# Optimization experiments

Hardware: AMD Instinct MI355X
Metric: run time of the kernel (lower is better)

## Reference

```python
import math
import jax, jax.numpy as jnp
import numpy as np

EPS = 1e-5
NUM_HEADER = 2


def pos_encoding(C, T, dtype):
    i = jnp.arange(C)
    exp = -((i - (i % 2)).astype(dtype) / C)
    freqs = jnp.power(jnp.asarray(10000.0, dtype), exp)[:, None]      # [C,1]
    phases = ((i % 2).astype(dtype) * (np.pi / 2))[:, None]           # [C,1]
    pos = jnp.arange(T, dtype=dtype)[None, :]                         # [1,T]
    return jnp.sin(pos * freqs + phases)                              # [C,T]


def layernorm2d(x, g, b):
    # LayerNorm over (C,T) jointly, per batch element (nn.LayerNorm([C, length]))
    mu = jnp.mean(x, axis=(1, 2), keepdims=True)
    var = jnp.mean((x - mu) ** 2, axis=(1, 2), keepdims=True)
    return (x - mu) * jax.lax.rsqrt(var + EPS) * g[None] + b[None]


def dsconv(x, dw_w, dw_b, pw_w, pw_b):
    # depthwise conv1d (groups=C, 'same' padding for odd k) + pointwise 1x1
    C = x.shape[1]
    k = dw_w.shape[-1]
    y = jax.lax.conv_general_dilated(
        x, dw_w[:, None, :], (1,), [(k // 2, k // 2)],
        dimension_numbers=('NCH', 'OIH', 'NCH'), feature_group_count=C)
    y = y + dw_b[None, :, None]
    y = jnp.einsum('bct,oc->bot', y, pw_w) + pw_b[None, :, None]
    return y


def attention(x, mask, Wq, Wk, Wv, Wo):
    # Faithful to source bug: all heads use Wqs[1]/Wks[1]/Wvs[1] -> identical heads.
    xt = jnp.transpose(x, (0, 2, 1))          # [B,T,C]
    C = xt.shape[-1]
    dk = C / NUM_HEADER
    q = xt @ Wq                               # [B,T,dk]
    k_ = xt @ Wk
    v = xt @ Wv
    s = jnp.einsum('bqd,bkd->bqk', q, k_) * (1.0 / math.sqrt(dk))
    hmask = mask[:, None, :]                  # mask over keys
    s = s * hmask + (1 - hmask) * (-1e30)
    a = jax.nn.softmax(s, axis=2) * mask[:, :, None]
    head = a @ v                              # [B,T,dk]
    heads = jnp.tile(head, (1, 1, NUM_HEADER))  # concat of identical heads
    out = heads @ Wo                          # [B,T,C]
    return jnp.transpose(out, (0, 2, 1))      # [B,C,T]


def setup_inputs() -> dict:
    key = jax.random.key(0)
    B, C, T = 16, 128, 1024
    NCONV, K = 4, 7
    dk = C // NUM_HEADER
    ks = jax.random.split(key, 12)
    inp = {
        'x': jax.random.normal(ks[0], (B, C, T), jnp.float32),
        'mask': jnp.ones((B, T), jnp.float32),
        'dw_w': jax.random.normal(ks[1], (NCONV, C, K), jnp.float32) * math.sqrt(2.0 / K),
        'dw_b': jnp.zeros((NCONV, C), jnp.float32),
        'pw_w': jax.random.normal(ks[2], (NCONV, C, C), jnp.float32) * math.sqrt(2.0 / C),
        'pw_b': jnp.zeros((NCONV, C), jnp.float32),
        'norm0_g': jnp.ones((C, T), jnp.float32),
        'norm0_b': jnp.zeros((C, T), jnp.float32),
        'norms_g': jnp.ones((NCONV, C, T), jnp.float32),
        'norms_b': jnp.zeros((NCONV, C, T), jnp.float32),
        'norme_g': jnp.ones((C, T), jnp.float32),
        'norme_b': jnp.zeros((C, T), jnp.float32),
        'Wq': jax.random.normal(ks[3], (C, dk), jnp.float32) * math.sqrt(2.0 / (C + dk)),
        'Wk': jax.random.normal(ks[4], (C, dk), jnp.float32) * math.sqrt(2.0 / (C + dk)),
        'Wv': jax.random.normal(ks[5], (C, dk), jnp.float32) * math.sqrt(2.0 / (C + dk)),
        'Wo': jax.random.normal(ks[6], (C, C), jnp.float32) * math.sqrt(2.0 / C),
        'fc_w': jax.random.normal(ks[7], (C, C), jnp.float32) * (0.1 * math.sqrt(6.0 / (2 * C))),
        'fc_b': jnp.zeros((C,), jnp.float32),
    }
    return inp


def reference(x, mask, dw_w, dw_b, pw_w, pw_b, norm0_g, norm0_b,
              norms_g, norms_b, norme_g, norme_b,
              Wq, Wk, Wv, Wo, fc_w, fc_b):
    B, C, T = x.shape
    nconv = dw_w.shape[0]
    # dropout is identity in eval mode (reference is deterministic)
    out = x + pos_encoding(C, T, x.dtype)[None]
    res = layernorm2d(out, norm0_g, norm0_b)
    for i in range(nconv):
        out = dsconv(out, dw_w[i], dw_b[i], pw_w[i], pw_b[i])
        out = jax.nn.relu(out)
        out = out + res
        res = out
        out = layernorm2d(out, norms_g[i], norms_b[i])
    out = attention(out, mask, Wq, Wk, Wv, Wo)
    out = out + res
    res = out
    out = layernorm2d(out, norme_g, norme_b)
    out = jnp.einsum('bct,oc->bot', out, fc_w) + fc_b[None, :, None]
    out = jax.nn.relu(out)
    out = out + res
    return out
```

## Files before the change

### kernel.cpp

```cpp
#include <hip/hip_runtime.h>
#include <math.h>

#define BB 16
#define CC 128
#define TT 1024
#define KK 7
#define DK 64
#define NSPLIT 4

typedef float f32x4 __attribute__((ext_vector_type(4)));
typedef short s16x8 __attribute__((ext_vector_type(8)));

__device__ inline short f2bf(float f) {
  union { float f; unsigned u; } v; v.f = f;
  unsigned r = (v.u + 0x7FFFu + ((v.u >> 16) & 1u)) >> 16;
  return (short)r;
}

__device__ inline void block_partial_256(float s, float ss, float* dst) {
#pragma unroll
  for (int off = 32; off; off >>= 1) { s += __shfl_xor(s, off); ss += __shfl_xor(ss, off); }
  __shared__ float red[8];
  int w = threadIdx.x >> 6;
  if ((threadIdx.x & 63) == 0) { red[2 * w] = s; red[2 * w + 1] = ss; }
  __syncthreads();
  if (threadIdx.x == 0) {
    for (int i = 1; i < 4; ++i) { s += red[2 * i]; ss += red[2 * i + 1]; }
    dst[0] = s; dst[1] = ss;
  }
}

__device__ inline void ln_stats_from_parts(const float* part_batch, int n, float* sh) {
  if (threadIdx.x < 64) {
    float s = 0.f, ss = 0.f;
    for (int i = threadIdx.x; i < n; i += 64) { s += part_batch[2 * i]; ss += part_batch[2 * i + 1]; }
#pragma unroll
    for (int off = 32; off; off >>= 1) { s += __shfl_xor(s, off); ss += __shfl_xor(ss, off); }
    if (threadIdx.x == 0) {
      const float invN = 1.f / (float)(CC * TT);
      float mu = s * invN;
      sh[0] = mu;
      sh[1] = rsqrtf(ss * invN - mu * mu + 1e-5f);
    }
  }
  __syncthreads();
}

__global__ __launch_bounds__(256) void k_prep(const float* __restrict__ pww,
                                              const float* __restrict__ Wq,
                                              const float* __restrict__ Wk,
                                              const float* __restrict__ Wv,
                                              const float* __restrict__ Wo,
                                              const float* __restrict__ fcw,
                                              short* __restrict__ pwwb,
                                              short* __restrict__ wqkvb,
                                              short* __restrict__ wo2b,
                                              short* __restrict__ fcwb) {
  int i = blockIdx.x * 256 + threadIdx.x;
  if (i < 65536) { pwwb[i] = f2bf(pww[i]); return; }
  i -= 65536;
  if (i < 24576) {
    int m = i >> 7, c = i & 127;
    int sel = m >> 6, d = m & 63;
    const float* srcp = sel == 0 ? Wq : (sel == 1 ? Wk : Wv);
    wqkvb[i] = f2bf(srcp[c * DK + d]);
    return;
  }
  i -= 24576;
  if (i < 8192) {
    int o = i >> 6, d = i & 63;
    wo2b[i] = f2bf(Wo[d * CC + o] + Wo[(d + 64) * CC + o]);
    return;
  }
  i -= 8192;
  fcwb[i] = f2bf(fcw[i]);
}

__global__ __launch_bounds__(256) void k_addpos(const float* __restrict__ x,
                                                float* __restrict__ out,
                                                float* __restrict__ part) {
  int bc = blockIdx.x;
  int c = bc & (CC - 1);
  float ce = (float)(c & ~1);
  float freq = expf(-(ce / (float)CC) * 9.210340371976184f);
  float phase = (c & 1) ? 1.5707963267948966f : 0.0f;
  const float* xr = x + (size_t)bc * TT;
  float* orow = out + (size_t)bc * TT;
  float s = 0.f, ss = 0.f;
  for (int t = threadIdx.x; t < TT; t += 256) {
    float v = xr[t] + sinf((float)t * freq + phase);
    orow[t] = v;
    s += v; ss += v * v;
  }
  block_partial_256(s, ss, part + (size_t)bc * 2);
}

template <bool LN_IN, bool LN_RES>
__global__ __launch_bounds__(256) void k_dsconv(const float* __restrict__ in,
                                                const float* __restrict__ lng,
                                                const float* __restrict__ lnb,
                                                const float* __restrict__ part_in, int npart,
                                                const float* __restrict__ dww,
                                                const float* __restrict__ dwb,
                                                const short* __restrict__ pwwb,
                                                const float* __restrict__ pwb,
                                                float* __restrict__ out,
                                                float* __restrict__ part_out) {
  int tile = blockIdx.x & 31, b = blockIdx.x >> 5;
  int t0 = tile * 32;
  __shared__ float stats[2];
  __shared__ float xs[CC][39];
  __shared__ __align__(16) short Dt[32][136];
  ln_stats_from_parts(part_in + (size_t)b * npart * 2, npart, stats);
  float mu = stats[0], rs = stats[1];

  for (int i = threadIdx.x; i < CC * 38; i += 256) {
    int c = i / 38, j = i - c * 38;
    int t = t0 + j - 3;
    float v = 0.f;
    if (t >= 0 && t < TT) {
      v = in[((size_t)b * CC + c) * TT + t];
      if (LN_IN) v = (v - mu) * rs * lng[c * TT + t] + lnb[c * TT + t];
    }
    xs[c][j] = v;
  }
  __syncthreads();
  for (int i = threadIdx.x; i < 32 * CC; i += 256) {
    int t = i >> 7, c = i & 127;
    float a = dwb[c];
#pragma unroll
    for (int j = 0; j < KK; ++j) a += dww[c * KK + j] * xs[c][t + j];
    Dt[t][c] = f2bf(a);
  }
  __syncthreads();

  int w = threadIdx.x >> 6, lane = threadIdx.x & 63;
  int lo = lane & 15, hi = lane >> 4;
  f32x4 acc[2][2];
#pragma unroll
  for (int mt = 0; mt < 2; ++mt)
#pragma unroll
    for (int nt = 0; nt < 2; ++nt) { acc[mt][nt][0] = 0.f; acc[mt][nt][1] = 0.f; acc[mt][nt][2] = 0.f; acc[mt][nt][3] = 0.f; }
#pragma unroll
  for (int ks = 0; ks < 4; ++ks) {
    s16x8 b0 = *(const s16x8*)&Dt[lo][ks * 32 + hi * 8];
    s16x8 b1 = *(const s16x8*)&Dt[16 + lo][ks * 32 + hi * 8];
    s16x8 a0 = *(const s16x8*)&pwwb[(size_t)(w * 32 + lo) * CC + ks * 32 + hi * 8];
    s16x8 a1 = *(const s16x8*)&pwwb[(size_t)(w * 32 + 16 + lo) * CC + ks * 32 + hi * 8];
    acc[0][0] = __builtin_amdgcn_mfma_f32_16x16x32_bf16(a0, b0, acc[0][0], 0, 0, 0);
    acc[0][1] = __builtin_amdgcn_mfma_f32_16x16x32_bf16(a0, b1, acc[0][1], 0, 0, 0);
    acc[1][0] = __builtin_amdgcn_mfma_f32_16x16x32_bf16(a1, b0, acc[1][0], 0, 0, 0);
    acc[1][1] = __builtin_amdgcn_mfma_f32_16x16x32_bf16(a1, b1, acc[1][1], 0, 0, 0);
  }

  float s = 0.f, ss = 0.f;
#pragma unroll
  for (int mt = 0; mt < 2; ++mt)
#pragma unroll
    for (int nt = 0; nt < 2; ++nt)
#pragma unroll
      for (int r = 0; r < 4; ++r) {
        int row = w * 32 + mt * 16 + hi * 4 + r;
        int t = t0 + nt * 16 + lo;
        float v = acc[mt][nt][r] + pwb[row];
        v = v > 0.f ? v : 0.f;
        size_t idx = ((size_t)b * CC + row) * TT + t;
        float rv = in[idx];
        if (LN_RES) rv = (rv - mu) * rs * lng[row * TT + t] + lnb[row * TT + t];
        v += rv;
        out[idx] = v;
        s += v; ss += v * v;
      }
  block_partial_256(s, ss, part_out + (size_t)blockIdx.x * 2);
}

__global__ __launch_bounds__(256) void k_qkv(const float* __restrict__ in,
                                             const float* __restrict__ lng,
                                             const float* __restrict__ lnb,
                                             const float* __restrict__ part_in,
                                             const short* __restrict__ wqkvb,
                                             short* __restrict__ q,
                                             short* __restrict__ k,
                                             short* __restrict__ vt) {
  int tile = blockIdx.x & 31, b = blockIdx.x >> 5;
  int t0 = tile * 32;
  __shared__ float stats[2];
  __shared__ __align__(16) short Dt[32][136];
  ln_stats_from_parts(part_in + (size_t)b * 64, 32, stats);
  float mu = stats[0], rs = stats[1];
  for (int i = threadIdx.x; i < CC * 32; i += 256) {
    int c = i >> 5, t = i & 31;
    float v = in[((size_t)b * CC + c) * TT + t0 + t];
    Dt[t][c] = f2bf((v - mu) * rs * lng[c * TT + t0 + t] + lnb[c * TT + t0 + t]);
  }
  __syncthreads();

  int w = threadIdx.x >> 6, lane = threadIdx.x & 63;
  int lo = lane & 15, hi = lane >> 4;
  f32x4 acc[3][2];
#pragma unroll
  for (int mt = 0; mt < 3; ++mt)
#pragma unroll
    for (int nt = 0; nt < 2; ++nt) { acc[mt][nt][0] = 0.f; acc[mt][nt][1] = 0.f; acc[mt][nt][2] = 0.f; acc[mt][nt][3] = 0.f; }
#pragma unroll
  for (int ks = 0; ks < 4; ++ks) {
    s16x8 b0 = *(const s16x8*)&Dt[lo][ks * 32 + hi * 8];
    s16x8 b1 = *(const s16x8*)&Dt[16 + lo][ks * 32 + hi * 8];
#pragma unroll
    for (int mt = 0; mt < 3; ++mt) {
      s16x8 a = *(const s16x8*)&wqkvb[(size_t)(w * 48 + mt * 16 + lo) * CC + ks * 32 + hi * 8];
      acc[mt][0] = __builtin_amdgcn_mfma_f32_16x16x32_bf16(a, b0, acc[mt][0], 0, 0, 0);
      acc[mt][1] = __builtin_amdgcn_mfma_f32_16x16x32_bf16(a, b1, acc[mt][1], 0, 0, 0);
    }
  }
#pragma unroll
  for (int mt = 0; mt < 3; ++mt)
#pragma unroll
    for (int nt = 0; nt < 2; ++nt) {
      int m0 = w * 48 + mt * 16 + hi * 4;
      int t = t0 + nt * 16 + lo;
      short4 pk;
      pk.x = f2bf(acc[mt][nt][0]); pk.y = f2bf(acc[mt][nt][1]);
      pk.z = f2bf(acc[mt][nt][2]); pk.w = f2bf(acc[mt][nt][3]);
      if (m0 < 64) {
        *(short4*)(q + ((size_t)b * TT + t) * DK + m0) = pk;
      } else if (m0 < 128) {
        *(short4*)(k + ((size_t)b * TT + t) * DK + (m0 - 64)) = pk;
      } else {
        int d = m0 - 128;
        vt[((size_t)b * DK + d) * TT + t] = pk.x;
        vt[((size_t)b * DK + d + 1) * TT + t] = pk.y;
        vt[((size_t)b * DK + d + 2) * TT + t] = pk.z;
        vt[((size_t)b * DK + d + 3) * TT + t] = pk.w;
      }
    }
}

__global__ __launch_bounds__(128) void k_attn(const short* __restrict__ qb,
                                              const short* __restrict__ kbuf,
                                              const short* __restrict__ vtb,
                                              const float* __restrict__ mask,
                                              float* __restrict__ pacc,
                                              float* __restrict__ pml) {
  int sp = blockIdx.x & (NSPLIT - 1);
  int qt = (blockIdx.x >> 2) & 31;
  int b = blockIdx.x >> 7;
  int w = threadIdx.x >> 6, lane = threadIdx.x & 63;
  int lo = lane & 15, hi = lane >> 4;

  __shared__ __align__(16) short ks[64][72];
  __shared__ __align__(16) short vt[64][72];
  __shared__ __align__(16) short ps[2][16][68];
  __shared__ float ms[64];

  const short* qp = qb + ((size_t)b * TT + qt * 32 + w * 16 + lo) * DK + hi * 8;
  s16x8 aq0 = *(const s16x8*)qp;
  s16x8 aq1 = *(const s16x8*)(qp + 32);

  f32x4 acc[4];
  float m_i[4], l_i[4];
#pragma unroll
  for (int r = 0; r < 4; ++r) {
    m_i[r] = -3.0e38f; l_i[r] = 0.f;
#pragma unroll
    for (int nt = 0; nt < 4; ++nt) acc[nt][r] = 0.f;
  }
  const float scale = 0.125f;

  for (int kb2 = sp * (TT / 64 / NSPLIT); kb2 < (sp + 1) * (TT / 64 / NSPLIT); ++kb2) {
    __syncthreads();
    for (int i = threadIdx.x; i < 512; i += 128) {
      int r = i >> 3, ch = i & 7;
      *(s16x8*)&ks[r][ch * 8] =
          *(const s16x8*)(kbuf + ((size_t)b * TT + kb2 * 64 + r) * DK + ch * 8);
      *(s16x8*)&vt[r][ch * 8] =
          *(const s16x8*)(vtb + ((size_t)b * DK + r) * TT + kb2 * 64 + ch * 8);
    }
    if (threadIdx.x < 64) ms[threadIdx.x] = mask[(size_t)b * TT + kb2 * 64 + threadIdx.x];
    __syncthreads();

    f32x4 sc[4];
#pragma unroll
    for (int nt = 0; nt < 4; ++nt) {
      f32x4 z; z[0] = 0.f; z[1] = 0.f; z[2] = 0.f; z[3] = 0.f;
      s16x8 bk0 = *(const s16x8*)&ks[nt * 16 + lo][hi * 8];
      s16x8 bk1 = *(const s16x8*)&ks[nt * 16 + lo][32 + hi * 8];
      z = __builtin_amdgcn_mfma_f32_16x16x32_bf16(aq0, bk0, z, 0, 0, 0);
      z = __builtin_amdgcn_mfma_f32_16x16x32_bf16(aq1, bk1, z, 0, 0, 0);
      sc[nt] = z;
    }
#pragma unroll
    for (int nt = 0; nt < 4; ++nt) {
      float mv = ms[nt * 16 + lo];
      float addv = (1.f - mv) * -1e30f;
#pragma unroll
      for (int r = 0; r < 4; ++r) sc[nt][r] = sc[nt][r] * scale * mv + addv;
    }
    float alpha[4];
#pragma unroll
    for (int r = 0; r < 4; ++r) {
      float m0 = fmaxf(fmaxf(sc[0][r], sc[1][r]), fmaxf(sc[2][r], sc[3][r]));
#pragma unroll
      for (int off = 1; off < 16; off <<= 1) m0 = fmaxf(m0, __shfl_xor(m0, off));
      float mn = fmaxf(m_i[r], m0);
      alpha[r] = __expf(m_i[r] - mn);
      m_i[r] = mn;
    }
    float psum[4] = {0.f, 0.f, 0.f, 0.f};
#pragma unroll
    for (int nt = 0; nt < 4; ++nt)
#pragma unroll
      for (int r = 0; r < 4; ++r) {
        float p = __expf(sc[nt][r] - m_i[r]);
        psum[r] += p;
        ps[w][hi * 4 + r][nt * 16 + lo] = f2bf(p);
      }
#pragma unroll
    for (int r = 0; r < 4; ++r) {
      float sum = psum[r];
#pragma unroll
      for (int off = 1; off < 16; off <<= 1) sum += __shfl_xor(sum, off);
      l_i[r] = l_i[r] * alpha[r] + sum;
    }
#pragma unroll
    for (int nt = 0; nt < 4; ++nt)
#pragma unroll
      for (int r = 0; r < 4; ++r) acc[nt][r] *= alpha[r];

    s16x8 ap0 = *(const s16x8*)&ps[w][lo][hi * 8];
    s16x8 ap1 = *(const s16x8*)&ps[w][lo][32 + hi * 8];
#pragma unroll
    for (int nt = 0; nt < 4; ++nt) {
      s16x8 bv0 = *(const s16x8*)&vt[nt * 16 + lo][hi * 8];
      s16x8 bv1 = *(const s16x8*)&vt[nt * 16 + lo][32 + hi * 8];
      acc[nt] = __builtin_amdgcn_mfma_f32_16x16x32_bf16(ap0, bv0, acc[nt], 0, 0, 0);
      acc[nt] = __builtin_amdgcn_mfma_f32_16x16x32_bf16(ap1, bv1, acc[nt], 0, 0, 0);
    }
  }
#pragma unroll
  for (int r = 0; r < 4; ++r) {
    int row = qt * 32 + w * 16 + hi * 4 + r;
    size_t pb = (((size_t)b * TT + row) * NSPLIT + sp) * DK;
#pragma unroll
    for (int nt = 0; nt < 4; ++nt) pacc[pb + nt * 16 + lo] = acc[nt][r];
    if (lo == 0) {
      size_t mb = (((size_t)b * TT + row) * NSPLIT + sp) * 2;
      pml[mb] = m_i[r];
      pml[mb + 1] = l_i[r];
    }
  }
}

__global__ __launch_bounds__(256) void k_attn_combine(const float* __restrict__ pacc,
                                                      const float* __restrict__ pml,
                                                      const float* __restrict__ mask,
                                                      short* __restrict__ head) {
  int tid = blockIdx.x * 256 + threadIdx.x;
  int chunk = tid & 3;
  int row = (tid >> 2) & (TT - 1);
  int b = tid >> 12;
  size_t rb = (size_t)b * TT + row;
  float m[NSPLIT], l[NSPLIT];
#pragma unroll
  for (int s = 0; s < NSPLIT; ++s) {
    m[s] = pml[(rb * NSPLIT + s) * 2];
    l[s] = pml[(rb * NSPLIT + s) * 2 + 1];
  }
  float M = fmaxf(fmaxf(m[0], m[1]), fmaxf(m[2], m[3]));
  float wgt[NSPLIT], L = 0.f;
#pragma unroll
  for (int s = 0; s < NSPLIT; ++s) { wgt[s] = __expf(m[s] - M); L += wgt[s] * l[s]; }
  float inv = mask[rb] / L;
  float o[16];
#pragma unroll
  for (int j = 0; j < 16; ++j) o[j] = 0.f;
#pragma unroll
  for (int s = 0; s < NSPLIT; ++s) {
    const float4* pa = (const float4*)(pacc + (rb * NSPLIT + s) * DK + chunk * 16);
#pragma unroll
    for (int j4 = 0; j4 < 4; ++j4) {
      float4 v = pa[j4];
      o[j4 * 4] += wgt[s] * v.x; o[j4 * 4 + 1] += wgt[s] * v.y;
      o[j4 * 4 + 2] += wgt[s] * v.z; o[j4 * 4 + 3] += wgt[s] * v.w;
    }
  }
  short h[16];
#pragma unroll
  for (int j = 0; j < 16; ++j) h[j] = f2bf(o[j] * inv);
  *(uint4*)(head + rb * DK + chunk * 16) = *(uint4*)h;
  *(uint4*)(head + rb * DK + chunk * 16 + 8) = *(uint4*)(h + 8);
}

__global__ __launch_bounds__(256) void k_attnout(const short* __restrict__ head,
                                                 const short* __restrict__ wo2b,
                                                 const float* __restrict__ res,
                                                 float* __restrict__ out,
                                                 float* __restrict__ part_out) {
  int tile = blockIdx.x & 31, b = blockIdx.x >> 5;
  int t0 = tile * 32;
  __shared__ __align__(16) short Ht[32][72];
  {
    int i = threadIdx.x;
    int t = i >> 3, ch = i & 7;
    *(s16x8*)&Ht[t][ch * 8] =
        *(const s16x8*)(head + ((size_t)b * TT + t0 + t) * DK + ch * 8);
  }
  __syncthreads();

  int w = threadIdx.x >> 6, lane = threadIdx.x & 63;
  int lo = lane & 15, hi = lane >> 4;
  f32x4 acc[2][2];
#pragma unroll
  for (int mt = 0; mt < 2; ++mt)
#pragma unroll
    for (int nt = 0; nt < 2; ++nt) { acc[mt][nt][0] = 0.f; acc[mt][nt][1] = 0.f; acc[mt][nt][2] = 0.f; acc[mt][nt][3] = 0.f; }
#pragma unroll
  for (int ks = 0; ks < 2; ++ks) {
    s16x8 b0 = *(const s16x8*)&Ht[lo][ks * 32 + hi * 8];
    s16x8 b1 = *(const s16x8*)&Ht[16 + lo][ks * 32 + hi * 8];
    s16x8 a0 = *(const s16x8*)&wo2b[(size_t)(w * 32 + lo) * DK + ks * 32 + hi * 8];
    s16x8 a1 = *(const s16x8*)&wo2b[(size_t)(w * 32 + 16 + lo) * DK + ks * 32 + hi * 8];
    acc[0][0] = __builtin_amdgcn_mfma_f32_16x16x32_bf16(a0, b0, acc[0][0], 0, 0, 0);
    acc[0][1] = __builtin_amdgcn_mfma_f32_16x16x32_bf16(a0, b1, acc[0][1], 0, 0, 0);
    acc[1][0] = __builtin_amdgcn_mfma_f32_16x16x32_bf16(a1, b0, acc[1][0], 0, 0, 0);
    acc[1][1] = __builtin_amdgcn_mfma_f32_16x16x32_bf16(a1, b1, acc[1][1], 0, 0, 0);
  }
  float s = 0.f, ss = 0.f;
#pragma unroll
  for (int mt = 0; mt < 2; ++mt)
#pragma unroll
    for (int nt = 0; nt < 2; ++nt)
#pragma unroll
      for (int r = 0; r < 4; ++r) {
        int row = w * 32 + mt * 16 + hi * 4 + r;
        int t = t0 + nt * 16 + lo;
        size_t idx = ((size_t)b * CC + row) * TT + t;
        float v = acc[mt][nt][r] + res[idx];
        out[idx] = v;
        s += v; ss += v * v;
      }
  block_partial_256(s, ss, part_out + (size_t)blockIdx.x * 2);
}

__global__ __launch_bounds__(256) void k_fc(const float* __restrict__ in,
                                            const float* __restrict__ lng,
                                            const float* __restrict__ lnb,
                                            const float* __restrict__ part_in,
                                            const short* __restrict__ fcwb,
                                            const float* __restrict__ fb,
                                            float* __restrict__ out) {
  int tile = blockIdx.x & 31, b = blockIdx.x >> 5;
  int t0 = tile * 32;
  __shared__ float stats[2];
  __shared__ __align__(16) short Dt[32][136];
  ln_stats_from_parts(part_in + (size_t)b * 64, 32, stats);
  float mu = stats[0], rs = stats[1];
  for (int i = threadIdx.x; i < CC * 32; i += 256) {
    int c = i >> 5, t = i & 31;
    float v = in[((size_t)b * CC + c) * TT + t0 + t];
    Dt[t][c] = f2bf((v - mu) * rs * lng[c * TT + t0 + t] + lnb[c * TT + t0 + t]);
  }
  __syncthreads();

  int w = threadIdx.x >> 6, lane = threadIdx.x & 63;
  int lo = lane & 15, hi = lane >> 4;
  f32x4 acc[2][2];
#pragma unroll
  for (int mt = 0; mt < 2; ++mt)
#pragma unroll
    for (int nt = 0; nt < 2; ++nt) { acc[mt][nt][0] = 0.f; acc[mt][nt][1] = 0.f; acc[mt][nt][2] = 0.f; acc[mt][nt][3] = 0.f; }
#pragma unroll
  for (int ks = 0; ks < 4; ++ks) {
    s16x8 b0 = *(const s16x8*)&Dt[lo][ks * 32 + hi * 8];
    s16x8 b1 = *(const s16x8*)&Dt[16 + lo][ks * 32 + hi * 8];
    s16x8 a0 = *(const s16x8*)&fcwb[(size_t)(w * 32 + lo) * CC + ks * 32 + hi * 8];
    s16x8 a1 = *(const s16x8*)&fcwb[(size_t)(w * 32 + 16 + lo) * CC + ks * 32 + hi * 8];
    acc[0][0] = __builtin_amdgcn_mfma_f32_16x16x32_bf16(a0, b0, acc[0][0], 0, 0, 0);
    acc[0][1] = __builtin_amdgcn_mfma_f32_16x16x32_bf16(a0, b1, acc[0][1], 0, 0, 0);
    acc[1][0] = __builtin_amdgcn_mfma_f32_16x16x32_bf16(a1, b0, acc[1][0], 0, 0, 0);
    acc[1][1] = __builtin_amdgcn_mfma_f32_16x16x32_bf16(a1, b1, acc[1][1], 0, 0, 0);
  }
#pragma unroll
  for (int mt = 0; mt < 2; ++mt)
#pragma unroll
    for (int nt = 0; nt < 2; ++nt)
#pragma unroll
      for (int r = 0; r < 4; ++r) {
        int row = w * 32 + mt * 16 + hi * 4 + r;
        int t = t0 + nt * 16 + lo;
        size_t idx = ((size_t)b * CC + row) * TT + t;
        float v = acc[mt][nt][r] + fb[row];
        v = v > 0.f ? v : 0.f;
        out[idx] = v + in[idx];
      }
}

extern "C" void kernel_launch(void* const* d_in, const int* in_sizes, int n_in,
                              void* d_out, int out_size, void* d_ws, size_t ws_size,
                              hipStream_t stream) {
  const float* x    = (const float*)d_in[0];
  const float* mask = (const float*)d_in[1];
  const float* dww  = (const float*)d_in[2];
  const float* dwb  = (const float*)d_in[3];
  const float* pww  = (const float*)d_in[4];
  const float* pwb  = (const float*)d_in[5];
  const float* n0g  = (const float*)d_in[6];
  const float* n0b  = (const float*)d_in[7];
  const float* nsg  = (const float*)d_in[8];
  const float* nsb  = (const float*)d_in[9];
  const float* neg_ = (const float*)d_in[10];
  const float* neb  = (const float*)d_in[11];
  const float* Wq   = (const float*)d_in[12];
  const float* Wk   = (const float*)d_in[13];
  const float* Wv   = (const float*)d_in[14];
  const float* Wo   = (const float*)d_in[15];
  const float* fcw  = (const float*)d_in[16];
  const float* fcb  = (const float*)d_in[17];
  float* out = (float*)d_out;

  float* W = (float*)d_ws;
  const size_t NBCT = (size_t)BB * CC * TT;
  const size_t NBTD = (size_t)BB * TT * DK;
  const size_t CT = (size_t)CC * TT;
  float* O     = W;
  float* S     = W + NBCT;
  float* PART0 = W + 2 * NBCT;
  float* PARTS = PART0 + 4096;
  float* PACC  = PARTS + 5 * 1024;
  float* PML   = PACC + NBTD * NSPLIT;
  short* QB    = (short*)(PML + (size_t)BB * TT * NSPLIT * 2);
  short* KB    = QB + NBTD;
  short* VT    = KB + NBTD;
  short* HDB   = VT + NBTD;
  short* PWWB  = HDB + NBTD;
  short* WQKVB = PWWB + 65536;
  short* WO2B  = WQKVB + 24576;
  short* FCWB  = WO2B + 8192;

  k_prep<<<448, 256, 0, stream>>>(pww, Wq, Wk, Wv, Wo, fcw, PWWB, WQKVB, WO2B, FCWB);
  k_addpos<<<BB * CC, 256, 0, stream>>>(x, O, PART0);
  k_dsconv<false, true><<<BB * 32, 256, 0, stream>>>(
      O, n0g, n0b, PART0, 128, dww, dwb, PWWB, pwb, S, PARTS);
  k_dsconv<true, false><<<BB * 32, 256, 0, stream>>>(
      S, nsg + 0 * CT, nsb + 0 * CT, PARTS, 32,
      dww + 1 * CC * KK, dwb + 1 * CC, PWWB + 1 * CC * CC, pwb + 1 * CC, O, PARTS + 1024);
  k_dsconv<true, false><<<BB * 32, 256, 0, stream>>>(
      O, nsg + 1 * CT, nsb + 1 * CT, PARTS + 1024, 32,
      dww + 2 * CC * KK, dwb + 2 * CC, PWWB + 2 * CC * CC, pwb + 2 * CC, S, PARTS + 2048);
  k_dsconv<true, false><<<BB * 32, 256, 0, stream>>>(
      S, nsg + 2 * CT, nsb + 2 * CT, PARTS + 2048, 32,
      dww + 3 * CC * KK, dwb + 3 * CC, PWWB + 3 * CC * CC, pwb + 3 * CC, O, PARTS + 3072);
  k_qkv<<<BB * 32, 256, 0, stream>>>(O, nsg + 3 * CT, nsb + 3 * CT, PARTS + 3072,
                                     WQKVB, QB, KB, VT);
  k_attn<<<BB * 32 * NSPLIT, 128, 0, stream>>>(QB, KB, VT, mask, PACC, PML);
  k_attn_combine<<<BB * TT * 4 / 256, 256, 0, stream>>>(PACC, PML, mask, HDB);
  k_attnout<<<BB * 32, 256, 0, stream>>>(HDB, WO2B, O, S, PARTS + 4096);
  k_fc<<<BB * 32, 256, 0, stream>>>(S, neg_, neb, PARTS + 4096, FCWB, fcb, out);
}
```

Before: 218.9 us.

## Fuse whole pipeline into one persistent megakernel with grid barriers

Replaces the chain of ten kernels with a single persistent kernel of 512 blocks. The blocks synchronise through atomic grid barriers. Each block keeps its [C,32] activation tile in shared memory across the conv layers, and neighbouring tiles trade only 4-column halos through a small global buffer. This removes the full-tensor global round trips and the per-launch overheads. Attention now runs in-block over two halves of the keys instead of a split-K kernel plus a combine kernel. The cost is that all blocks must be co-resident for the spin barriers, and the conv, QKV, attention and FC stages can no longer be tuned separately for occupancy.

```diff
diff --git a/kernel.cpp b/kernel.cpp
--- a/kernel.cpp
+++ b/kernel.cpp
@@ -6,7 +6,7 @@
 #define TT 1024
 #define KK 7
 #define DK 64
-#define NSPLIT 4
+#define NBLK 512
 
 typedef float f32x4 __attribute__((ext_vector_type(4)));
 typedef short s16x8 __attribute__((ext_vector_type(8)));
@@ -30,10 +30,10 @@
   }
 }
 
-__device__ inline void ln_stats_from_parts(const float* part_batch, int n, float* sh) {
+__device__ inline void ln_stats32(const float* part, float* sh) {
   if (threadIdx.x < 64) {
     float s = 0.f, ss = 0.f;
-    for (int i = threadIdx.x; i < n; i += 64) { s += part_batch[2 * i]; ss += part_batch[2 * i + 1]; }
+    if (threadIdx.x < 32) { s = part[2 * threadIdx.x]; ss = part[2 * threadIdx.x + 1]; }
 #pragma unroll
     for (int off = 32; off; off >>= 1) { s += __shfl_xor(s, off); ss += __shfl_xor(ss, off); }
     if (threadIdx.x == 0) {
@@ -46,453 +46,473 @@
   __syncthreads();
 }
 
-__global__ __launch_bounds__(256) void k_prep(const float* __restrict__ pww,
-                                              const float* __restrict__ Wq,
-                                              const float* __restrict__ Wk,
-                                              const float* __restrict__ Wv,
-                                              const float* __restrict__ Wo,
-                                              const float* __restrict__ fcw,
-                                              short* __restrict__ pwwb,
-                                              short* __restrict__ wqkvb,
-                                              short* __restrict__ wo2b,
-                                              short* __restrict__ fcwb) {
-  int i = blockIdx.x * 256 + threadIdx.x;
-  if (i < 65536) { pwwb[i] = f2bf(pww[i]); return; }
-  i -= 65536;
-  if (i < 24576) {
-    int m = i >> 7, c = i & 127;
-    int sel = m >> 6, d = m & 63;
-    const float* srcp = sel == 0 ? Wq : (sel == 1 ? Wk : Wv);
-    wqkvb[i] = f2bf(srcp[c * DK + d]);
-    return;
-  }
-  i -= 24576;
-  if (i < 8192) {
-    int o = i >> 6, d = i & 63;
-    wo2b[i] = f2bf(Wo[d * CC + o] + Wo[(d + 64) * CC + o]);
-    return;
-  }
-  i -= 8192;
-  fcwb[i] = f2bf(fcw[i]);
+__device__ inline void gridbar(unsigned* cnt, int idx) {
+  __threadfence();
+  __syncthreads();
+  if (threadIdx.x == 0) {
+    unsigned prev = __hip_atomic_fetch_add(&cnt[idx], 1u, __ATOMIC_ACQ_REL, __HIP_MEMORY_SCOPE_AGENT);
+    if (prev != (unsigned)(NBLK - 1)) {
+      while (__hip_atomic_load(&cnt[idx], __ATOMIC_ACQUIRE, __HIP_MEMORY_SCOPE_AGENT) < (unsigned)NBLK)
+        __builtin_amdgcn_s_sleep(2);
+    }
+  }
+  __syncthreads();
+  __threadfence();
 }
 
-__global__ __launch_bounds__(256) void k_addpos(const float* __restrict__ x,
-                                                float* __restrict__ out,
-                                                float* __restrict__ part) {
-  int bc = blockIdx.x;
-  int c = bc & (CC - 1);
-  float ce = (float)(c & ~1);
-  float freq = expf(-(ce / (float)CC) * 9.210340371976184f);
-  float phase = (c & 1) ? 1.5707963267948966f : 0.0f;
-  const float* xr = x + (size_t)bc * TT;
-  float* orow = out + (size_t)bc * TT;
-  float s = 0.f, ss = 0.f;
-  for (int t = threadIdx.x; t < TT; t += 256) {
-    float v = xr[t] + sinf((float)t * freq + phase);
-    orow[t] = v;
-    s += v; ss += v * v;
-  }
-  block_partial_256(s, ss, part + (size_t)bc * 2);
-}
-
-template <bool LN_IN, bool LN_RES>
-__global__ __launch_bounds__(256) void k_dsconv(const float* __restrict__ in,
-                                                const float* __restrict__ lng,
-                                                const float* __restrict__ lnb,
-                                                const float* __restrict__ part_in, int npart,
-                                                const float* __restrict__ dww,
-                                                const float* __restrict__ dwb,
-                                                const short* __restrict__ pwwb,
-                                                const float* __restrict__ pwb,
-                                                float* __restrict__ out,
-                                                float* __restrict__ part_out) {
-  int tile = blockIdx.x & 31, b = blockIdx.x >> 5;
-  int t0 = tile * 32;
+struct SmemDs {
+  float xs[CC][41];
+  float dwl[CC][9];
+  float dwb2[CC];
+  short Dt[32][136];
+};
+struct SmemAtHalf {
+  short ks[64][72];
+  short vt[64][72];
+  short ps[2][16][68];
+  float ms[64];
+};
+struct SmemAt {
+  SmemAtHalf h[2];
+  short Ht[32][72];
+};
+union Smem { SmemDs ds; SmemAt at; };
+
+__global__ __launch_bounds__(256, 2) void k_mega(
+    const float* __restrict__ x, const float* __restrict__ mask,
+    const float* __restrict__ dww, const float* __restrict__ dwb,
+    const float* __restrict__ pww, const float* __restrict__ pwb,
+    const float* __restrict__ n0g, const float* __restrict__ n0b,
+    const float* __restrict__ nsg, const float* __restrict__ nsb,
+    const float* __restrict__ neg_, const float* __restrict__ neb,
+    const float* __restrict__ Wq, const float* __restrict__ Wk,
+    const float* __restrict__ Wv, const float* __restrict__ Wo,
+    const float* __restrict__ fcw, const float* __restrict__ fcb,
+    float* __restrict__ out,
+    float* __restrict__ PART, float* __restrict__ HB,
+    short* __restrict__ KB, short* __restrict__ VT,
+    short* __restrict__ PWWB, short* __restrict__ WQKVB,
+    short* __restrict__ WO2B, short* __restrict__ FCWB,
+    unsigned* __restrict__ CNT) {
+  __shared__ Smem S_;
+  __shared__ float cur[CC][33];
+  __shared__ short Qs[32][72];
   __shared__ float stats[2];
-  __shared__ float xs[CC][39];
-  __shared__ __align__(16) short Dt[32][136];
-  ln_stats_from_parts(part_in + (size_t)b * npart * 2, npart, stats);
-  float mu = stats[0], rs = stats[1];
-
-  for (int i = threadIdx.x; i < CC * 38; i += 256) {
-    int c = i / 38, j = i - c * 38;
-    int t = t0 + j - 3;
-    float v = 0.f;
-    if (t >= 0 && t < TT) {
-      v = in[((size_t)b * CC + c) * TT + t];
-      if (LN_IN) v = (v - mu) * rs * lng[c * TT + t] + lnb[c * TT + t];
-    }
-    xs[c][j] = v;
-  }
-  __syncthreads();
-  for (int i = threadIdx.x; i < 32 * CC; i += 256) {
-    int t = i >> 7, c = i & 127;
-    float a = dwb[c];
-#pragma unroll
-    for (int j = 0; j < KK; ++j) a += dww[c * KK + j] * xs[c][t + j];
-    Dt[t][c] = f2bf(a);
-  }
-  __syncthreads();
-
-  int w = threadIdx.x >> 6, lane = threadIdx.x & 63;
-  int lo = lane & 15, hi = lane >> 4;
-  f32x4 acc[2][2];
-#pragma unroll
-  for (int mt = 0; mt < 2; ++mt)
-#pragma unroll
-    for (int nt = 0; nt < 2; ++nt) { acc[mt][nt][0] = 0.f; acc[mt][nt][1] = 0.f; acc[mt][nt][2] = 0.f; acc[mt][nt][3] = 0.f; }
-#pragma unroll
-  for (int ks = 0; ks < 4; ++ks) {
-    s16x8 b0 = *(const s16x8*)&Dt[lo][ks * 32 + hi * 8];
-    s16x8 b1 = *(const s16x8*)&Dt[16 + lo][ks * 32 + hi * 8];
-    s16x8 a0 = *(const s16x8*)&pwwb[(size_t)(w * 32 + lo) * CC + ks * 32 + hi * 8];
-    s16x8 a1 = *(const s16x8*)&pwwb[(size_t)(w * 32 + 16 + lo) * CC + ks * 32 + hi * 8];
-    acc[0][0] = __builtin_amdgcn_mfma_f32_16x16x32_bf16(a0, b0, acc[0][0], 0, 0, 0);
-    acc[0][1] = __builtin_amdgcn_mfma_f32_16x16x32_bf16(a0, b1, acc[0][1], 0, 0, 0);
-    acc[1][0] = __builtin_amdgcn_mfma_f32_16x16x32_bf16(a1, b0, acc[1][0], 0, 0, 0);
-    acc[1][1] = __builtin_amdgcn_mfma_f32_16x16x32_bf16(a1, b1, acc[1][1], 0, 0, 0);
-  }
-
-  float s = 0.f, ss = 0.f;
-#pragma unroll
-  for (int mt = 0; mt < 2; ++mt)
-#pragma unroll
-    for (int nt = 0; nt < 2; ++nt)
+
+  const int tid = threadIdx.x;
+  const int bid = blockIdx.x;
+  const int b = bid >> 5, tile = bid & 31, t0 = tile * 32;
+  const size_t CT = (size_t)CC * TT;
+
+  const int w4 = tid >> 6;
+  const int lane = tid & 63;
+  const int lo = lane & 15, hi = lane >> 4;
+
+  {
+    int i = bid * 256 + tid;
+    if (i < 65536) {
+      PWWB[i] = f2bf(pww[i]);
+    } else if (i < 90112) {
+      int j = i - 65536;
+      int m = j >> 7, c = j & 127;
+      int sel = m >> 6, d = m & 63;
+      const float* srcp = sel == 0 ? Wq : (sel == 1 ? Wk : Wv);
+      WQKVB[j] = f2bf(srcp[c * DK + d]);
+    } else if (i < 98304) {
+      int j = i - 90112;
+      int o = j >> 6, d = j & 63;
+      WO2B[j] = f2bf(Wo[d * CC + o] + Wo[(d + 64) * CC + o]);
+    } else if (i < 114688) {
+      int j = i - 98304;
+      FCWB[j] = f2bf(fcw[j]);
+    }
+  }
+  {
+    float s = 0.f, ss = 0.f;
+    for (int u = tid; u < 1024; u += 256) {
+      int c = u >> 3, q = u & 7;
+      int t = t0 + q * 4;
+      float4 v = *(const float4*)(x + ((size_t)b * CC + c) * TT + t);
+      float ce = (float)(c & ~1);
+      float freq = expf(-(ce * (1.f / (float)CC)) * 9.210340371976184f);
+      float ph = (c & 1) ? 1.5707963267948966f : 0.f;
+      v.x += sinf((float)(t + 0) * freq + ph);
+      v.y += sinf((float)(t + 1) * freq + ph);
+      v.z += sinf((float)(t + 2) * freq + ph);
+      v.w += sinf((float)(t + 3) * freq + ph);
+      int tl = q * 4;
+      cur[c][tl] = v.x; cur[c][tl + 1] = v.y; cur[c][tl + 2] = v.z; cur[c][tl + 3] = v.w;
+      if (q == 0) *(float4*)&HB[((size_t)bid * CC + c) * 8] = v;
+      if (q == 7) *(float4*)&HB[((size_t)bid * CC + c) * 8 + 4] = v;
+      s += v.x + v.y + v.z + v.w;
+      ss += v.x * v.x + v.y * v.y + v.z * v.z + v.w * v.w;
+    }
+    block_partial_256(s, ss, PART + (size_t)bid * 2);
+  }
+  gridbar(CNT, 0);
+
+  for (int it = 0; it < 4; ++it) {
+    ln_stats32(PART + (size_t)it * 1024 + b * 64, stats);
+    float mu = stats[0], rs = stats[1];
+    const bool lnin = (it > 0);
+    const float* g  = lnin ? (nsg + (size_t)(it - 1) * CT) : n0g;
+    const float* bb = lnin ? (nsb + (size_t)(it - 1) * CT) : n0b;
+    const float* Hin = HB + (size_t)it * 524288;
+    float* Hout = HB + (size_t)(it + 1) * 524288;
+
+    for (int i = tid; i < CC * KK; i += 256) {
+      int c = i / KK;
+      S_.ds.dwl[c][i - c * KK] = dww[(size_t)it * CC * KK + i];
+    }
+    if (tid < CC) S_.ds.dwb2[tid] = dwb[it * CC + tid];
+
+    for (int u = tid; u < 1024; u += 256) {
+      int c = u >> 3, q = u & 7;
+      int j0 = 4 + q * 4, tl = q * 4;
+      float v0 = cur[c][tl], v1 = cur[c][tl + 1], v2 = cur[c][tl + 2], v3 = cur[c][tl + 3];
+      if (lnin) {
+        size_t off = (size_t)c * TT + t0 + tl;
+        float4 gg = *(const float4*)(g + off);
+        float4 b4 = *(const float4*)(bb + off);
+        v0 = (v0 - mu) * rs * gg.x + b4.x;
+        v1 = (v1 - mu) * rs * gg.y + b4.y;
+        v2 = (v2 - mu) * rs * gg.z + b4.z;
+        v3 = (v3 - mu) * rs * gg.w + b4.w;
+      }
+      S_.ds.xs[c][j0] = v0; S_.ds.xs[c][j0 + 1] = v1;
+      S_.ds.xs[c][j0 + 2] = v2; S_.ds.xs[c][j0 + 3] = v3;
+    }
+    {
+      int c = tid >> 1, sd = tid & 1;
+      int jb = sd ? 36 : 0;
+      int tb = sd ? (t0 + 32) : (t0 - 4);
+      float h0 = 0.f, h1 = 0.f, h2 = 0.f, h3 = 0.f;
+      if (tb >= 0 && tb < TT) {
+        int ntile = sd ? tile + 1 : tile - 1;
+        float4 h4 = *(const float4*)&Hin[(((size_t)b * 32 + ntile) * CC + c) * 8 + (sd ? 0 : 4)];
+        h0 = h4.x; h1 = h4.y; h2 = h4.z; h3 = h4.w;
+        if (lnin) {
+          size_t off = (size_t)c * TT + tb;
+          h0 = (h0 - mu) * rs * g[off] + bb[off];
+          h1 = (h1 - mu) * rs * g[off + 1] + bb[off + 1];
+          h2 = (h2 - mu) * rs * g[off + 2] + bb[off + 2];
+          h3 = (h3 - mu) * rs * g[off + 3] + bb[off + 3];
+        }
+      }
+      S_.ds.xs[c][jb] = h0; S_.ds.xs[c][jb + 1] = h1;
+      S_.ds.xs[c][jb + 2] = h2; S_.ds.xs[c][jb + 3] = h3;
+    }
+    __syncthreads();
+    for (int i = tid; i < 32 * CC; i += 256) {
+      int t = i >> 7, c = i & 127;
+      float a = S_.ds.dwb2[c];
+#pragma unroll
+      for (int j = 0; j < KK; ++j) a += S_.ds.dwl[c][j] * S_.ds.xs[c][t + j + 1];
+      S_.ds.Dt[t][c] = f2bf(a);
+    }
+    __syncthreads();
+    const short* pwp = PWWB + (size_t)it * CC * CC;
+    f32x4 acc[2][2];
+#pragma unroll
+    for (int mt = 0; mt < 2; ++mt)
+#pragma unroll
+      for (int nt = 0; nt < 2; ++nt) { acc[mt][nt][0] = 0.f; acc[mt][nt][1] = 0.f; acc[mt][nt][2] = 0.f; acc[mt][nt][3] = 0.f; }
+#pragma unroll
+    for (int ks = 0; ks < 4; ++ks) {
+      s16x8 b0 = *(const s16x8*)&S_.ds.Dt[lo][ks * 32 + hi * 8];
+      s16x8 b1 = *(const s16x8*)&S_.ds.Dt[16 + lo][ks * 32 + hi * 8];
+      s16x8 a0 = *(const s16x8*)&pwp[(size_t)(w4 * 32 + lo) * CC + ks * 32 + hi * 8];
+      s16x8 a1 = *(const s16x8*)&pwp[(size_t)(w4 * 32 + 16 + lo) * CC + ks * 32 + hi * 8];
+      acc[0][0] = __builtin_amdgcn_mfma_f32_16x16x32_bf16(a0, b0, acc[0][0], 0, 0, 0);
+      acc[0][1] = __builtin_amdgcn_mfma_f32_16x16x32_bf16(a0, b1, acc[0][1], 0, 0, 0);
+      acc[1][0] = __builtin_amdgcn_mfma_f32_16x16x32_bf16(a1, b0, acc[1][0], 0, 0, 0);
+      acc[1][1] = __builtin_amdgcn_mfma_f32_16x16x32_bf16(a1, b1, acc[1][1], 0, 0, 0);
+    }
+    float s = 0.f, ss = 0.f;
+#pragma unroll
+    for (int mt = 0; mt < 2; ++mt)
+#pragma unroll
+      for (int nt = 0; nt < 2; ++nt)
+#pragma unroll
+        for (int r = 0; r < 4; ++r) {
+          int row = w4 * 32 + mt * 16 + hi * 4 + r;
+          int tl = nt * 16 + lo;
+          float v = acc[mt][nt][r] + pwb[it * CC + row];
+          v = v > 0.f ? v : 0.f;
+          float rv;
+          if (it == 0) {
+            size_t off = (size_t)row * TT + t0 + tl;
+            rv = (cur[row][tl] - mu) * rs * n0g[off] + n0b[off];
+          } else {
+            rv = cur[row][tl];
+          }
+          v += rv;
+          cur[row][tl] = v;
+          if (it < 3) {
+            if (tl < 4) Hout[((size_t)bid * CC + row) * 8 + tl] = v;
+            else if (tl >= 28) Hout[((size_t)bid * CC + row) * 8 + tl - 24] = v;
+          }
+          s += v; ss += v * v;
+        }
+    block_partial_256(s, ss, PART + (size_t)(it + 1) * 1024 + bid * 2);
+    gridbar(CNT, 1 + it);
+  }
+
+  {
+    ln_stats32(PART + 4 * 1024 + b * 64, stats);
+    float mu = stats[0], rs = stats[1];
+    const float* g = nsg + 3 * CT;
+    const float* bb = nsb + 3 * CT;
+    for (int u = tid; u < 1024; u += 256) {
+      int c = u >> 3, q = u & 7;
+      int t = q * 4;
+      size_t off = (size_t)c * TT + t0 + t;
+      float4 gg = *(const float4*)(g + off);
+      float4 b4 = *(const float4*)(bb + off);
+      S_.ds.Dt[t + 0][c] = f2bf((cur[c][t + 0] - mu) * rs * gg.x + b4.x);
+      S_.ds.Dt[t + 1][c] = f2bf((cur[c][t + 1] - mu) * rs * gg.y + b4.y);
+      S_.ds.Dt[t + 2][c] = f2bf((cur[c][t + 2] - mu) * rs * gg.z + b4.z);
+      S_.ds.Dt[t + 3][c] = f2bf((cur[c][t + 3] - mu) * rs * gg.w + b4.w);
+    }
+    __syncthreads();
+    f32x4 acc[3][2];
+#pragma unroll
+    for (int mt = 0; mt < 3; ++mt)
+#pragma unroll
+      for (int nt = 0; nt < 2; ++nt) { acc[mt][nt][0] = 0.f; acc[mt][nt][1] = 0.f; acc[mt][nt][2] = 0.f; acc[mt][nt][3] = 0.f; }
+#pragma unroll
+    for (int ks = 0; ks < 4; ++ks) {
+      s16x8 b0 = *(const s16x8*)&S_.ds.Dt[lo][ks * 32 + hi * 8];
+      s16x8 b1 = *(const s16x8*)&S_.ds.Dt[16 + lo][ks * 32 + hi * 8];
+#pragma unroll
+      for (int mt = 0; mt < 3; ++mt) {
+        s16x8 a = *(const s16x8*)&WQKVB[(size_t)(w4 * 48 + mt * 16 + lo) * CC + ks * 32 + hi * 8];
+        acc[mt][0] = __builtin_amdgcn_mfma_f32_16x16x32_bf16(a, b0, acc[mt][0], 0, 0, 0);
+        acc[mt][1] = __builtin_amdgcn_mfma_f32_16x16x32_bf16(a, b1, acc[mt][1], 0, 0, 0);
+      }
+    }
+#pragma unroll
+    for (int mt = 0; mt < 3; ++mt)
+#pragma unroll
+      for (int nt = 0; nt < 2; ++nt) {
+        int m0 = w4 * 48 + mt * 16 + hi * 4;
+        int tl = nt * 16 + lo;
+        int t = t0 + tl;
+        short4 pk;
+        pk.x = f2bf(acc[mt][nt][0]); pk.y = f2bf(acc[mt][nt][1]);
+        pk.z = f2bf(acc[mt][nt][2]); pk.w = f2bf(acc[mt][nt][3]);
+        if (m0 < 64) {
+          *(short4*)&Qs[tl][m0] = pk;
+        } else if (m0 < 128) {
+          *(short4*)(KB + ((size_t)b * TT + t) * DK + (m0 - 64)) = pk;
+        } else {
+          int d = m0 - 128;
+          VT[((size_t)b * DK + d) * TT + t] = pk.x;
+          VT[((size_t)b * DK + d + 1) * TT + t] = pk.y;
+          VT[((size_t)b * DK + d + 2) * TT + t] = pk.z;
+          VT[((size_t)b * DK + d + 3) * TT + t] = pk.w;
+        }
+      }
+    gridbar(CNT, 5);
+  }
+
+  {
+    const int half = tid >> 7;
+    const int ltid = tid & 127;
+    const int hw = ltid >> 6;
+    SmemAtHalf& A = S_.at.h[half];
+
+    s16x8 aq0 = *(const s16x8*)&Qs[hw * 16 + lo][hi * 8];
+    s16x8 aq1 = *(const s16x8*)&Qs[hw * 16 + lo][32 + hi * 8];
+
+    f32x4 acc[4];
+    float m_i[4], l_i[4];
+#pragma unroll
+    for (int r = 0; r < 4; ++r) {
+      m_i[r] = -3.0e38f; l_i[r] = 0.f;
+#pragma unroll
+      for (int nt = 0; nt < 4; ++nt) acc[nt][r] = 0.f;
+    }
+    const float scale = 0.125f;
+
+    for (int it2 = 0; it2 < 8; ++it2) {
+      int kb2 = half * 8 + it2;
+      __syncthreads();
+      for (int i = ltid; i < 512; i += 128) {
+        int r = i >> 3, ch = i & 7;
+        *(s16x8*)&A.ks[r][ch * 8] =
+            *(const s16x8*)(KB + ((size_t)b * TT + kb2 * 64 + r) * DK + ch * 8);
+        *(s16x8*)&A.vt[r][ch * 8] =
+            *(const s16x8*)(VT + ((size_t)b * DK + r) * TT + kb2 * 64 + ch * 8);
+      }
+      if (ltid < 64) A.ms[ltid] = mask[(size_t)b * TT + kb2 * 64 + ltid];
+      __syncthreads();
+
+      f32x4 sc[4];
+#pragma unroll
+      for (int nt = 0; nt < 4; ++nt) {
+        f32x4 z; z[0] = 0.f; z[1] = 0.f; z[2] = 0.f; z[3] = 0.f;
+        s16x8 bk0 = *(const s16x8*)&A.ks[nt * 16 + lo][hi * 8];
+        s16x8 bk1 = *(const s16x8*)&A.ks[nt * 16 + lo][32 + hi * 8];
+        z = __builtin_amdgcn_mfma_f32_16x16x32_bf16(aq0, bk0, z, 0, 0, 0);
+        z = __builtin_amdgcn_mfma_f32_16x16x32_bf16(aq1, bk1, z, 0, 0, 0);
+        sc[nt] = z;
+      }
+#pragma unroll
+      for (int nt = 0; nt < 4; ++nt) {
+        float mv = A.ms[nt * 16 + lo];
+        float addv = (1.f - mv) * -1e30f;
+#pragma unroll
+        for (int r = 0; r < 4; ++r) sc[nt][r] = sc[nt][r] * scale * mv + addv;
+      }
+      float alpha[4];
 #pragma unroll
       for (int r = 0; r < 4; ++r) {
-        int row = w * 32 + mt * 16 + hi * 4 + r;
-        int t = t0 + nt * 16 + lo;
-        float v = acc[mt][nt][r] + pwb[row];
-        v = v > 0.f ? v : 0.f;
-        size_t idx = ((size_t)b * CC + row) * TT + t;
-        float rv = in[idx];
-        if (LN_RES) rv = (rv - mu) * rs * lng[row * TT + t] + lnb[row * TT + t];
-        v += rv;
-        out[idx] = v;
-        s += v; ss += v * v;
-      }
-  block_partial_256(s, ss, part_out + (size_t)blockIdx.x * 2);
-}
-
-__global__ __launch_bounds__(256) void k_qkv(const float* __restrict__ in,
-                                             const float* __restrict__ lng,
-                                             const float* __restrict__ lnb,
-                                             const float* __restrict__ part_in,
-                                             const short* __restrict__ wqkvb,
-                                             short* __restrict__ q,
-                                             short* __restrict__ k,
-                                             short* __restrict__ vt) {
-  int tile = blockIdx.x & 31, b = blockIdx.x >> 5;
-  int t0 = tile * 32;
-  __shared__ float stats[2];
-  __shared__ __align__(16) short Dt[32][136];
-  ln_stats_from_parts(part_in + (size_t)b * 64, 32, stats);
-  float mu = stats[0], rs = stats[1];
-  for (int i = threadIdx.x; i < CC * 32; i += 256) {
-    int c = i >> 5, t = i & 31;
-    float v = in[((size_t)b * CC + c) * TT + t0 + t];
-    Dt[t][c] = f2bf((v - mu) * rs * lng[c * TT + t0 + t] + lnb[c * TT + t0 + t]);
-  }
-  __syncthreads();
-
-  int w = threadIdx.x >> 6, lane = threadIdx.x & 63;
-  int lo = lane & 15, hi = lane >> 4;
-  f32x4 acc[3][2];
-#pragma unroll
-  for (int mt = 0; mt < 3; ++mt)
-#pragma unroll
-    for (int nt = 0; nt < 2; ++nt) { acc[mt][nt][0] = 0.f; acc[mt][nt][1] = 0.f; acc[mt][nt][2] = 0.f; acc[mt][nt][3] = 0.f; }
-#pragma unroll
-  for (int ks = 0; ks < 4; ++ks) {
-    s16x8 b0 = *(const s16x8*)&Dt[lo][ks * 32 + hi * 8];
-    s16x8 b1 = *(const s16x8*)&Dt[16 + lo][ks * 32 + hi * 8];
-#pragma unroll
-    for (int mt = 0; mt < 3; ++mt) {
-      s16x8 a = *(const s16x8*)&wqkvb[(size_t)(w * 48 + mt * 16 + lo) * CC + ks * 32 + hi * 8];
-      acc[mt][0] = __builtin_amdgcn_mfma_f32_16x16x32_bf16(a, b0, acc[mt][0], 0, 0, 0);
-      acc[mt][1] = __builtin_amdgcn_mfma_f32_16x16x32_bf16(a, b1, acc[mt][1], 0, 0, 0);
-    }
-  }
-#pragma unroll
-  for (int mt = 0; mt < 3; ++mt)
-#pragma unroll
-    for (int nt = 0; nt < 2; ++nt) {
-      int m0 = w * 48 + mt * 16 + hi * 4;
-      int t = t0 + nt * 16 + lo;
-      short4 pk;
-      pk.x = f2bf(acc[mt][nt][0]); pk.y = f2bf(acc[mt][nt][1]);
-      pk.z = f2bf(acc[mt][nt][2]); pk.w = f2bf(acc[mt][nt][3]);
-      if (m0 < 64) {
-        *(short4*)(q + ((size_t)b * TT + t) * DK + m0) = pk;
-      } else if (m0 < 128) {
-        *(short4*)(k + ((size_t)b * TT + t) * DK + (m0 - 64)) = pk;
-      } else {
-        int d = m0 - 128;
-        vt[((size_t)b * DK + d) * TT + t] = pk.x;
-        vt[((size_t)b * DK + d + 1) * TT + t] = pk.y;
-        vt[((size_t)b * DK + d + 2) * TT + t] = pk.z;
-        vt[((size_t)b * DK + d + 3) * TT + t] = pk.w;
-      }
-    }
-}
-
-__global__ __launch_bounds__(128) void k_attn(const short* __restrict__ qb,
-                                              const short* __restrict__ kbuf,
-                                              const short* __restrict__ vtb,
-                                              const float* __restrict__ mask,
-                                              float* __restrict__ pacc,
-                                              float* __restrict__ pml) {
-  int sp = blockIdx.x & (NSPLIT - 1);
-  int qt = (blockIdx.x >> 2) & 31;
-  int b = blockIdx.x >> 7;
-  int w = threadIdx.x >> 6, lane = threadIdx.x & 63;
-  int lo = lane & 15, hi = lane >> 4;
-
-  __shared__ __align__(16) short ks[64][72];
-  __shared__ __align__(16) short vt[64][72];
-  __shared__ __align__(16) short ps[2][16][68];
-  __shared__ float ms[64];
-
-  const short* qp = qb + ((size_t)b * TT + qt * 32 + w * 16 + lo) * DK + hi * 8;
-  s16x8 aq0 = *(const s16x8*)qp;
-  s16x8 aq1 = *(const s16x8*)(qp + 32);
-
-  f32x4 acc[4];
-  float m_i[4], l_i[4];
-#pragma unroll
-  for (int r = 0; r < 4; ++r) {
-    m_i[r] = -3.0e38f; l_i[r] = 0.f;
-#pragma unroll
-    for (int nt = 0; nt < 4; ++nt) acc[nt][r] = 0.f;
-  }
-  const float scale = 0.125f;
-
-  for (int kb2 = sp * (TT / 64 / NSPLIT); kb2 < (sp + 1) * (TT / 64 / NSPLIT); ++kb2) {
-    __syncthreads();
-    for (int i = threadIdx.x; i < 512; i += 128) {
-      int r = i >> 3, ch = i & 7;
-      *(s16x8*)&ks[r][ch * 8] =
-          *(const s16x8*)(kbuf + ((size_t)b * TT + kb2 * 64 + r) * DK + ch * 8);
-      *(s16x8*)&vt[r][ch * 8] =
-          *(const s16x8*)(vtb + ((size_t)b * DK + r) * TT + kb2 * 64 + ch * 8);
-    }
-    if (threadIdx.x < 64) ms[threadIdx.x] = mask[(size_t)b * TT + kb2 * 64 + threadIdx.x];
-    __syncthreads();
-
-    f32x4 sc[4];
-#pragma unroll
-    for (int nt = 0; nt < 4; ++nt) {
-      f32x4 z; z[0] = 0.f; z[1] = 0.f; z[2] = 0.f; z[3] = 0.f;
-      s16x8 bk0 = *(const s16x8*)&ks[nt * 16 + lo][hi * 8];
-      s16x8 bk1 = *(const s16x8*)&ks[nt * 16 + lo][32 + hi * 8];
-      z = __builtin_amdgcn_mfma_f32_16x16x32_bf16(aq0, bk0, z, 0, 0, 0);
-      z = __builtin_amdgcn_mfma_f32_16x16x32_bf16(aq1, bk1, z, 0, 0, 0);
-      sc[nt] = z;
-    }
-#pragma unroll
-    for (int nt = 0; nt < 4; ++nt) {
-      float mv = ms[nt * 16 + lo];
-      float addv = (1.f - mv) * -1e30f;
-#pragma unroll
-      for (int r = 0; r < 4; ++r) sc[nt][r] = sc[nt][r] * scale * mv + addv;
-    }
-    float alpha[4];
-#pragma unroll
-    for (int r = 0; r < 4; ++r) {
-      float m0 = fmaxf(fmaxf(sc[0][r], sc[1][r]), fmaxf(sc[2][r], sc[3][r]));
-#pragma unroll
-      for (int off = 1; off < 16; off <<= 1) m0 = fmaxf(m0, __shfl_xor(m0, off));
-      float mn = fmaxf(m_i[r], m0);
-      alpha[r] = __expf(m_i[r] - mn);
-      m_i[r] = mn;
-    }
-    float psum[4] = {0.f, 0.f, 0.f, 0.f};
-#pragma unroll
-    for (int nt = 0; nt < 4; ++nt)
+        float m0 = fmaxf(fmaxf(sc[0][r], sc[1][r]), fmaxf(sc[2][r], sc[3][r]));
+#pragma unroll
+        for (int off = 1; off < 16; off <<= 1) m0 = fmaxf(m0, __shfl_xor(m0, off));
+        float mn = fmaxf(m_i[r], m0);
+        alpha[r] = __expf(m_i[r] - mn);
+        m_i[r] = mn;
+      }
+      float psum[4] = {0.f, 0.f, 0.f, 0.f};
+#pragma unroll
+      for (int nt = 0; nt < 4; ++nt)
+#pragma unroll
+        for (int r = 0; r < 4; ++r) {
+          float p = __expf(sc[nt][r] - m_i[r]);
+          psum[r] += p;
+          A.ps[hw][hi * 4 + r][nt * 16 + lo] = f2bf(p);
+        }
 #pragma unroll
       for (int r = 0; r < 4; ++r) {
-        float p = __expf(sc[nt][r] - m_i[r]);
-        psum[r] += p;
-        ps[w][hi * 4 + r][nt * 16 + lo] = f2bf(p);
-      }
-#pragma unroll
-    for (int r = 0; r < 4; ++r) {
-      float sum = psum[r];
-#pragma unroll
-      for (int off = 1; off < 16; off <<= 1) sum += __shfl_xor(sum, off);
-      l_i[r] = l_i[r] * alpha[r] + sum;
-    }
-#pragma unroll
-    for (int nt = 0; nt < 4; ++nt)
-#pragma unroll
-      for (int r = 0; r < 4; ++r) acc[nt][r] *= alpha[r];
-
-    s16x8 ap0 = *(const s16x8*)&ps[w][lo][hi * 8];
-    s16x8 ap1 = *(const s16x8*)&ps[w][lo][32 + hi * 8];
-#pragma unroll
-    for (int nt = 0; nt < 4; ++nt) {
-      s16x8 bv0 = *(const s16x8*)&vt[nt * 16 + lo][hi * 8];
-      s16x8 bv1 = *(const s16x8*)&vt[nt * 16 + lo][32 + hi * 8];
-      acc[nt] = __builtin_amdgcn_mfma_f32_16x16x32_bf16(ap0, bv0, acc[nt], 0, 0, 0);
-      acc[nt] = __builtin_amdgcn_mfma_f32_16x16x32_bf16(ap1, bv1, acc[nt], 0, 0, 0);
-    }
-  }
-#pragma unroll
-  for (int r = 0; r < 4; ++r) {
-    int row = qt * 32 + w * 16 + hi * 4 + r;
-    size_t pb = (((size_t)b * TT + row) * NSPLIT + sp) * DK;
-#pragma unroll
-    for (int nt = 0; nt < 4; ++nt) pacc[pb + nt * 16 + lo] = acc[nt][r];
-    if (lo == 0) {
-      size_t mb = (((size_t)b * TT + row) * NSPLIT + sp) * 2;
-      pml[mb] = m_i[r];
-      pml[mb + 1] = l_i[r];
-    }
-  }
-}
-
-__global__ __launch_bounds__(256) void k_attn_combine(const float* __restrict__ pacc,
-                                                      const float* __restrict__ pml,
-                                                      const float* __restrict__ mask,
-                                                      short* __restrict__ head) {
-  int tid = blockIdx.x * 256 + threadIdx.x;
-  int chunk = tid & 3;
-  int row = (tid >> 2) & (TT - 1);
-  int b = tid >> 12;
-  size_t rb = (size_t)b * TT + row;
-  float m[NSPLIT], l[NSPLIT];
-#pragma unroll
-  for (int s = 0; s < NSPLIT; ++s) {
-    m[s] = pml[(rb * NSPLIT + s) * 2];
-    l[s] = pml[(rb * NSPLIT + s) * 2 + 1];
-  }
-  float M = fmaxf(fmaxf(m[0], m[1]), fmaxf(m[2], m[3]));
-  float wgt[NSPLIT], L = 0.f;
-#pragma unroll
-  for (int s = 0; s < NSPLIT; ++s) { wgt[s] = __expf(m[s] - M); L += wgt[s] * l[s]; }
-  float inv = mask[rb] / L;
-  float o[16];
-#pragma unroll
-  for (int j = 0; j < 16; ++j) o[j] = 0.f;
-#pragma unroll
-  for (int s = 0; s < NSPLIT; ++s) {
-    const float4* pa = (const float4*)(pacc + (rb * NSPLIT + s) * DK + chunk * 16);
-#pragma unroll
-    for (int j4 = 0; j4 < 4; ++j4) {
-      float4 v = pa[j4];
-      o[j4 * 4] += wgt[s] * v.x; o[j4 * 4 + 1] += wgt[s] * v.y;
-      o[j4 * 4 + 2] += wgt[s] * v.z; o[j4 * 4 + 3] += wgt[s] * v.w;
-    }
-  }
-  short h[16];
-#pragma unroll
-  for (int j = 0; j < 16; ++j) h[j] = f2bf(o[j] * inv);
-  *(uint4*)(head + rb * DK + chunk * 16) = *(uint4*)h;
-  *(uint4*)(head + rb * DK + chunk * 16 + 8) = *(uint4*)(h + 8);
-}
-
-__global__ __launch_bounds__(256) void k_attnout(const short* __restrict__ head,
-                                                 const short* __restrict__ wo2b,
-                                                 const float* __restrict__ res,
-                                                 float* __restrict__ out,
-                                                 float* __restrict__ part_out) {
-  int tile = blockIdx.x & 31, b = blockIdx.x >> 5;
-  int t0 = tile * 32;
-  __shared__ __align__(16) short Ht[32][72];
+        float sum = psum[r];
+#pragma unroll
+        for (int off = 1; off < 16; off <<= 1) sum += __shfl_xor(sum, off);
+        l_i[r] = l_i[r] * alpha[r] + sum;
+      }
+#pragma unroll
+      for (int nt = 0; nt < 4; ++nt)
+#pragma unroll
+        for (int r = 0; r < 4; ++r) acc[nt][r] *= alpha[r];
+
+      s16x8 ap0 = *(const s16x8*)&A.ps[hw][lo][hi * 8];
+      s16x8 ap1 = *(const s16x8*)&A.ps[hw][lo][32 + hi * 8];
+#pragma unroll
+      for (int nt = 0; nt < 4; ++nt) {
+        s16x8 bv0 = *(const s16x8*)&A.vt[nt * 16 + lo][hi * 8];
+        s16x8 bv1 = *(const s16x8*)&A.vt[nt * 16 + lo][32 + hi * 8];
+        acc[nt] = __builtin_amdgcn_mfma_f32_16x16x32_bf16(ap0, bv0, acc[nt], 0, 0, 0);
+        acc[nt] = __builtin_amdgcn_mfma_f32_16x16x32_bf16(ap1, bv1, acc[nt], 0, 0, 0);
+      }
+    }
+    __syncthreads();
+    float* cmb = (float*)&S_.at.h[0];
+    float* ml1 = (float*)&S_.at.h[1];
+    if (half == 1) {
+#pragma unroll
+      for (int r = 0; r < 4; ++r) {
+        int row = hw * 16 + hi * 4 + r;
+#pragma unroll
+        for (int nt = 0; nt < 4; ++nt) cmb[row * 64 + nt * 16 + lo] = acc[nt][r];
+        if (lo == 0) { ml1[row * 2] = m_i[r]; ml1[row * 2 + 1] = l_i[r]; }
+      }
+    }
+    __syncthreads();
+    if (half == 0) {
+#pragma unroll
+      for (int r = 0; r < 4; ++r) {
+        int row = hw * 16 + hi * 4 + r;
+        float m1 = ml1[row * 2], l1 = ml1[row * 2 + 1];
+        float M = fmaxf(m_i[r], m1);
+        float w0 = __expf(m_i[r] - M), w1 = __expf(m1 - M);
+        float L = w0 * l_i[r] + w1 * l1;
+        float inv = mask[(size_t)b * TT + t0 + row] / L;
+#pragma unroll
+        for (int nt = 0; nt < 4; ++nt)
+          S_.at.Ht[row][nt * 16 + lo] =
+              f2bf((w0 * acc[nt][r] + w1 * cmb[row * 64 + nt * 16 + lo]) * inv);
+      }
+    }
+    __syncthreads();
+    f32x4 acc2[2][2];
+#pragma unroll
+    for (int mt = 0; mt < 2; ++mt)
+#pragma unroll
+      for (int nt = 0; nt < 2; ++nt) { acc2[mt][nt][0] = 0.f; acc2[mt][nt][1] = 0.f; acc2[mt][nt][2] = 0.f; acc2[mt][nt][3] = 0.f; }
+#pragma unroll
+    for (int ks = 0; ks < 2; ++ks) {
+      s16x8 b0 = *(const s16x8*)&S_.at.Ht[lo][ks * 32 + hi * 8];
+      s16x8 b1 = *(const s16x8*)&S_.at.Ht[16 + lo][ks * 32 + hi * 8];
+      s16x8 a0 = *(const s16x8*)&WO2B[(size_t)(w4 * 32 + lo) * DK + ks * 32 + hi * 8];
+      s16x8 a1 = *(const s16x8*)&WO2B[(size_t)(w4 * 32 + 16 + lo) * DK + ks * 32 + hi * 8];
+      acc2[0][0] = __builtin_amdgcn_mfma_f32_16x16x32_bf16(a0, b0, acc2[0][0], 0, 0, 0);
+      acc2[0][1] = __builtin_amdgcn_mfma_f32_16x16x32_bf16(a0, b1, acc2[0][1], 0, 0, 0);
+      acc2[1][0] = __builtin_amdgcn_mfma_f32_16x16x32_bf16(a1, b0, acc2[1][0], 0, 0, 0);
+      acc2[1][1] = __builtin_amdgcn_mfma_f32_16x16x32_bf16(a1, b1, acc2[1][1], 0, 0, 0);
+    }
+    float s = 0.f, ss = 0.f;
+#pragma unroll
+    for (int mt = 0; mt < 2; ++mt)
+#pragma unroll
+      for (int nt = 0; nt < 2; ++nt)
+#pragma unroll
+        for (int r = 0; r < 4; ++r) {
+          int row = w4 * 32 + mt * 16 + hi * 4 + r;
+          int tl = nt * 16 + lo;
+          float v = acc2[mt][nt][r] + cur[row][tl];
+          cur[row][tl] = v;
+          s += v; ss += v * v;
+        }
+    block_partial_256(s, ss, PART + 5 * 1024 + (size_t)bid * 2);
+    gridbar(CNT, 6);
+  }
+
   {
-    int i = threadIdx.x;
-    int t = i >> 3, ch = i & 7;
-    *(s16x8*)&Ht[t][ch * 8] =
-        *(const s16x8*)(head + ((size_t)b * TT + t0 + t) * DK + ch * 8);
-  }
-  __syncthreads();
-
-  int w = threadIdx.x >> 6, lane = threadIdx.x & 63;
-  int lo = lane & 15, hi = lane >> 4;
-  f32x4 acc[2][2];
-#pragma unroll
-  for (int mt = 0; mt < 2; ++mt)
-#pragma unroll
-    for (int nt = 0; nt < 2; ++nt) { acc[mt][nt][0] = 0.f; acc[mt][nt][1] = 0.f; acc[mt][nt][2] = 0.f; acc[mt][nt][3] = 0.f; }
-#pragma unroll
-  for (int ks = 0; ks < 2; ++ks) {
-    s16x8 b0 = *(const s16x8*)&Ht[lo][ks * 32 + hi * 8];
-    s16x8 b1 = *(const s16x8*)&Ht[16 + lo][ks * 32 + hi * 8];
-    s16x8 a0 = *(const s16x8*)&wo2b[(size_t)(w * 32 + lo) * DK + ks * 32 + hi * 8];
-    s16x8 a1 = *(const s16x8*)&wo2b[(size_t)(w * 32 + 16 + lo) * DK + ks * 32 + hi * 8];
-    acc[0][0] = __builtin_amdgcn_mfma_f32_16x16x32_bf16(a0, b0, acc[0][0], 0, 0, 0);
-    acc[0][1] = __builtin_amdgcn_mfma_f32_16x16x32_bf16(a0, b1, acc[0][1], 0, 0, 0);
-    acc[1][0] = __builtin_amdgcn_mfma_f32_16x16x32_bf16(a1, b0, acc[1][0], 0, 0, 0);
-    acc[1][1] = __builtin_amdgcn_mfma_f32_16x16x32_bf16(a1, b1, acc[1][1], 0, 0, 0);
-  }
-  float s = 0.f, ss = 0.f;
-#pragma unroll
-  for (int mt = 0; mt < 2; ++mt)
-#pragma unroll
-    for (int nt = 0; nt < 2; ++nt)
-#pragma unroll
-      for (int r = 0; r < 4; ++r) {
-        int row = w * 32 + mt * 16 + hi * 4 + r;
-        int t = t0 + nt * 16 + lo;
-        size_t idx = ((size_t)b * CC + row) * TT + t;
-        float v = acc[mt][nt][r] + res[idx];
-        out[idx] = v;
-        s += v; ss += v * v;
-      }
-  block_partial_256(s, ss, part_out + (size_t)blockIdx.x * 2);
-}
-
-__global__ __launch_bounds__(256) void k_fc(const float* __restrict__ in,
-                                            const float* __restrict__ lng,
-                                            const float* __restrict__ lnb,
-                                            const float* __restrict__ part_in,
-                                            const short* __restrict__ fcwb,
-                                            const float* __restrict__ fb,
-                                            float* __restrict__ out) {
-  int tile = blockIdx.x & 31, b = blockIdx.x >> 5;
-  int t0 = tile * 32;
-  __shared__ float stats[2];
-  __shared__ __align__(16) short Dt[32][136];
-  ln_stats_from_parts(part_in + (size_t)b * 64, 32, stats);
-  float mu = stats[0], rs = stats[1];
-  for (int i = threadIdx.x; i < CC * 32; i += 256) {
-    int c = i >> 5, t = i & 31;
-    float v = in[((size_t)b * CC + c) * TT + t0 + t];
-    Dt[t][c] = f2bf((v - mu) * rs * lng[c * TT + t0 + t] + lnb[c * TT + t0 + t]);
-  }
-  __syncthreads();
-
-  int w = threadIdx.x >> 6, lane = threadIdx.x & 63;
-  int lo = lane & 15, hi = lane >> 4;
-  f32x4 acc[2][2];
-#pragma unroll
-  for (int mt = 0; mt < 2; ++mt)
-#pragma unroll
-    for (int nt = 0; nt < 2; ++nt) { acc[mt][nt][0] = 0.f; acc[mt][nt][1] = 0.f; acc[mt][nt][2] = 0.f; acc[mt][nt][3] = 0.f; }
-#pragma unroll
-  for (int ks = 0; ks < 4; ++ks) {
-    s16x8 b0 = *(const s16x8*)&Dt[lo][ks * 32 + hi * 8];
-    s16x8 b1 = *(const s16x8*)&Dt[16 + lo][ks * 32 + hi * 8];
-    s16x8 a0 = *(const s16x8*)&fcwb[(size_t)(w * 32 + lo) * CC + ks * 32 + hi * 8];
-    s16x8 a1 = *(const s16x8*)&fcwb[(size_t)(w * 32 + 16 + lo) * CC + ks * 32 + hi * 8];
-    acc[0][0] = __builtin_amdgcn_mfma_f32_16x16x32_bf16(a0, b0, acc[0][0], 0, 0, 0);
-    acc[0][1] = __builtin_amdgcn_mfma_f32_16x16x32_bf16(a0, b1, acc[0][1], 0, 0, 0);
-    acc[1][0] = __builtin_amdgcn_mfma_f32_16x16x32_bf16(a1, b0, acc[1][0], 0, 0, 0);
-    acc[1][1] = __builtin_amdgcn_mfma_f32_16x16x32_bf16(a1, b1, acc[1][1], 0, 0, 0);
-  }
-#pragma unroll
-  for (int mt = 0; mt < 2; ++mt)
-#pragma unroll
-    for (int nt = 0; nt < 2; ++nt)
-#pragma unroll
-      for (int r = 0; r < 4; ++r) {
-        int row = w * 32 + mt * 16 + hi * 4 + r;
-        int t = t0 + nt * 16 + lo;
-        size_t idx = ((size_t)b * CC + row) * TT + t;
-        float v = acc[mt][nt][r] + fb[row];
-        v = v > 0.f ? v : 0.f;
-        out[idx] = v + in[idx];
-      }
+    ln_stats32(PART + 5 * 1024 + b * 64, stats);
+    float mu = stats[0], rs = stats[1];
+    for (int u = tid; u < 1024; u += 256) {
+      int c = u >> 3, q = u & 7;
+      int t = q * 4;
+      size_t off = (size_t)c * TT + t0 + t;
+      float4 gg = *(const float4*)(neg_ + off);
+      float4 b4 = *(const float4*)(neb + off);
+      S_.ds.Dt[t + 0][c] = f2bf((cur[c][t + 0] - mu) * rs * gg.x + b4.x);
+      S_.ds.Dt[t + 1][c] = f2bf((cur[c][t + 1] - mu) * rs * gg.y + b4.y);
+      S_.ds.Dt[t + 2][c] = f2bf((cur[c][t + 2] - mu) * rs * gg.z + b4.z);
+      S_.ds.Dt[t + 3][c] = f2bf((cur[c][t + 3] - mu) * rs * gg.w + b4.w);
+    }
+    __syncthreads();
+    f32x4 acc[2][2];
+#pragma unroll
+    for (int mt = 0; mt < 2; ++mt)
+#pragma unroll
+      for (int nt = 0; nt < 2; ++nt) { acc[mt][nt][0] = 0.f; acc[mt][nt][1] = 0.f; acc[mt][nt][2] = 0.f; acc[mt][nt][3] = 0.f; }
+#pragma unroll
+    for (int ks = 0; ks < 4; ++ks) {
+      s16x8 b0 = *(const s16x8*)&S_.ds.Dt[lo][ks * 32 + hi * 8];
+      s16x8 b1 = *(const s16x8*)&S_.ds.Dt[16 + lo][ks * 32 + hi * 8];
+      s16x8 a0 = *(const s16x8*)&FCWB[(size_t)(w4 * 32 + lo) * CC + ks * 32 + hi * 8];
+      s16x8 a1 = *(const s16x8*)&FCWB[(size_t)(w4 * 32 + 16 + lo) * CC + ks * 32 + hi * 8];
+      acc[0][0] = __builtin_amdgcn_mfma_f32_16x16x32_bf16(a0, b0, acc[0][0], 0, 0, 0);
+      acc[0][1] = __builtin_amdgcn_mfma_f32_16x16x32_bf16(a0, b1, acc[0][1], 0, 0, 0);
+      acc[1][0] = __builtin_amdgcn_mfma_f32_16x16x32_bf16(a1, b0, acc[1][0], 0, 0, 0);
+      acc[1][1] = __builtin_amdgcn_mfma_f32_16x16x32_bf16(a1, b1, acc[1][1], 0, 0, 0);
+    }
+#pragma unroll
+    for (int mt = 0; mt < 2; ++mt)
+#pragma unroll
+      for (int nt = 0; nt < 2; ++nt)
+#pragma unroll
+        for (int r = 0; r < 4; ++r) {
+          int row = w4 * 32 + mt * 16 + hi * 4 + r;
+          int tl = nt * 16 + lo;
+          size_t idx = ((size_t)b * CC + row) * TT + t0 + tl;
+          float v = acc[mt][nt][r] + fcb[row];
+          v = v > 0.f ? v : 0.f;
+          out[idx] = v + cur[row][tl];
+        }
+  }
 }
 
 extern "C" void kernel_launch(void* const* d_in, const int* in_sizes, int n_in,
@@ -518,42 +538,20 @@
   const float* fcb  = (const float*)d_in[17];
   float* out = (float*)d_out;
 
+  const size_t NBTD = (size_t)BB * TT * DK;
   float* W = (float*)d_ws;
-  const size_t NBCT = (size_t)BB * CC * TT;
-  const size_t NBTD = (size_t)BB * TT * DK;
-  const size_t CT = (size_t)CC * TT;
-  float* O     = W;
-  float* S     = W + NBCT;
-  float* PART0 = W + 2 * NBCT;
-  float* PARTS = PART0 + 4096;
-  float* PACC  = PARTS + 5 * 1024;
-  float* PML   = PACC + NBTD * NSPLIT;
-  short* QB    = (short*)(PML + (size_t)BB * TT * NSPLIT * 2);
-  short* KB    = QB + NBTD;
+  float* PART = W;
+  float* HB   = W + 8192;
+  unsigned* CNT = (unsigned*)(W + 8192 + 4 * 524288);
+  short* KB    = (short*)(CNT + 32);
   short* VT    = KB + NBTD;
-  short* HDB   = VT + NBTD;
-  short* PWWB  = HDB + NBTD;
+  short* PWWB  = VT + NBTD;
   short* WQKVB = PWWB + 65536;
   short* WO2B  = WQKVB + 24576;
   short* FCWB  = WO2B + 8192;
 
-  k_prep<<<448, 256, 0, stream>>>(pww, Wq, Wk, Wv, Wo, fcw, PWWB, WQKVB, WO2B, FCWB);
-  k_addpos<<<BB * CC, 256, 0, stream>>>(x, O, PART0);
-  k_dsconv<false, true><<<BB * 32, 256, 0, stream>>>(
-      O, n0g, n0b, PART0, 128, dww, dwb, PWWB, pwb, S, PARTS);
-  k_dsconv<true, false><<<BB * 32, 256, 0, stream>>>(
-      S, nsg + 0 * CT, nsb + 0 * CT, PARTS, 32,
-      dww + 1 * CC * KK, dwb + 1 * CC, PWWB + 1 * CC * CC, pwb + 1 * CC, O, PARTS + 1024);
-  k_dsconv<true, false><<<BB * 32, 256, 0, stream>>>(
-      O, nsg + 1 * CT, nsb + 1 * CT, PARTS + 1024, 32,
-      dww + 2 * CC * KK, dwb + 2 * CC, PWWB + 2 * CC * CC, pwb + 2 * CC, S, PARTS + 2048);
-  k_dsconv<true, false><<<BB * 32, 256, 0, stream>>>(
-      S, nsg + 2 * CT, nsb + 2 * CT, PARTS + 2048, 32,
-      dww + 3 * CC * KK, dwb + 3 * CC, PWWB + 3 * CC * CC, pwb + 3 * CC, O, PARTS + 3072);
-  k_qkv<<<BB * 32, 256, 0, stream>>>(O, nsg + 3 * CT, nsb + 3 * CT, PARTS + 3072,
-                                     WQKVB, QB, KB, VT);
-  k_attn<<<BB * 32 * NSPLIT, 128, 0, stream>>>(QB, KB, VT, mask, PACC, PML);
-  k_attn_combine<<<BB * TT * 4 / 256, 256, 0, stream>>>(PACC, PML, mask, HDB);
-  k_attnout<<<BB * 32, 256, 0, stream>>>(HDB, WO2B, O, S, PARTS + 4096);
-  k_fc<<<BB * 32, 256, 0, stream>>>(S, neg_, neb, PARTS + 4096, FCWB, fcb, out);
+  hipMemsetAsync(CNT, 0, 32 * sizeof(unsigned), stream);
+  k_mega<<<NBLK, 256, 0, stream>>>(x, mask, dww, dwb, pww, pwb, n0g, n0b, nsg, nsb,
+                                   neg_, neb, Wq, Wk, Wv, Wo, fcw, fcb, out,
+                                   PART, HB, KB, VT, PWWB, WQKVB, WO2B, FCWB, CNT);
 }
```

Measured after the change: 831.1 us. 280% more time.
